# Kernel tuning notes

Hardware: AMD Instinct MI355X
Metric: run time of the kernel (lower is better)

The kernel has to match this reference:

```python
import jax, jax.numpy as jnp
import numpy as np

BATCH, SEQ, H_IN, N_STATE, H_OUT = 16, 4096, 128, 256, 128
RMIN, RMAX, MAX_PHASE = 0.9, 1.0, 6.283


def setup_inputs() -> dict:
    key = jax.random.key(0)
    ks = jax.random.split(key, 9)
    u = jax.random.normal(ks[0], (BATCH, SEQ, H_IN), jnp.float32)
    # LRU exponential parameterization init (matches torch __init__)
    u1 = jax.random.uniform(ks[1], (N_STATE,), jnp.float32)
    u2 = jax.random.uniform(ks[2], (N_STATE,), jnp.float32)
    nu_log = jnp.log(-0.5 * jnp.log(u1 * (RMAX + RMIN) * (RMAX - RMIN) + RMIN ** 2))
    theta_log = jnp.log(MAX_PHASE * u2)
    lam_abs = jnp.exp(-jnp.exp(nu_log))
    gamma_log = jnp.log(jnp.sqrt(1.0 - lam_abs ** 2))
    s2in = np.sqrt(2.0 * H_IN).astype(np.float32)
    B_re = jax.random.normal(ks[3], (N_STATE, H_IN), jnp.float32) / s2in
    B_im = jax.random.normal(ks[4], (N_STATE, H_IN), jnp.float32) / s2in
    sst = np.sqrt(float(N_STATE)).astype(np.float32)
    C_re = jax.random.normal(ks[5], (H_OUT, N_STATE), jnp.float32) / sst
    C_im = jax.random.normal(ks[6], (H_OUT, N_STATE), jnp.float32) / sst
    D = jax.random.normal(ks[7], (H_OUT, H_IN), jnp.float32) / np.sqrt(float(H_IN)).astype(np.float32)
    return dict(u=u, nu_log=nu_log, theta_log=theta_log, gamma_log=gamma_log,
                B_re=B_re, B_im=B_im, C_re=C_re, C_im=C_im, D=D)


def _combine(a, b):
    # complex affine composition: (l, x) o (l', x') -> (l*l', l'*x + x')
    l1r, l1i, x1r, x1i = a
    l2r, l2i, x2r, x2i = b
    lr = l1r * l2r - l1i * l2i
    li = l1r * l2i + l1i * l2r
    xr = l2r * x1r - l2i * x1i + x2r
    xi = l2r * x1i + l2i * x1r + x2i
    return (lr, li, xr, xi)


def reference(u, nu_log, theta_log, gamma_log, B_re, B_im, C_re, C_im, D):
    lam_mod = jnp.exp(-jnp.exp(nu_log))          # |lambda|, [N]
    th = jnp.exp(theta_log)
    lam_re = lam_mod * jnp.cos(th)
    lam_im = lam_mod * jnp.sin(th)
    gammas = jnp.exp(gamma_log)                  # [N]
    # input projection Bu_t = gamma * (B @ u_t), complex -> real/imag parts
    Bu_re = jnp.einsum('blh,nh->bln', u, B_re) * gammas  # [B,L,N]
    Bu_im = jnp.einsum('blh,nh->bln', u, B_im) * gammas
    Bsz, L, N = Bu_re.shape
    lr = jnp.broadcast_to(lam_re, (Bsz, L, N))
    li = jnp.broadcast_to(lam_im, (Bsz, L, N))
    # parallel scan of x_t = lambda * x_{t-1} + Bu_t, x0 = 0
    _, _, xr, xi = jax.lax.associative_scan(_combine, (lr, li, Bu_re, Bu_im), axis=1)
    zero = jnp.zeros((Bsz, 1, N), u.dtype)
    pre_re = jnp.concatenate([zero, xr[:, :-1]], axis=1)  # states[:, :-1]
    pre_im = jnp.concatenate([zero, xi[:, :-1]], axis=1)
    # y_t = Re(C x_{t-1}) + D u_t
    y = (jnp.einsum('bln,on->blo', pre_re, C_re)
         - jnp.einsum('bln,on->blo', pre_im, C_im)
         + jnp.einsum('blh,oh->blo', u, D))
    return y
```

## Files before the change

### kernel.cpp

```cpp
#include <hip/hip_runtime.h>
#include <math.h>

#define BATCH 16
#define SEQ   4096
#define HIN   128
#define NST   256
#define HOUT  128
#define CL    32
#define NC    (SEQ/CL)
#define ROWS  (BATCH*SEQ)
#define KTOT  640
#define NPRE  512

typedef __attribute__((ext_vector_type(8))) short short8;
typedef __attribute__((ext_vector_type(4))) float f32x4;

__device__ inline unsigned short f2bf(float f) {
  union { float f; unsigned u; } v; v.f = f;
  unsigned r = v.u + 0x7FFFu + ((v.u >> 16) & 1u);
  return (unsigned short)(r >> 16);
}
__device__ inline float bf2f(unsigned short s) {
  union { unsigned u; float f; } v; v.u = ((unsigned)s) << 16;
  return v.f;
}
__device__ inline float bits2f(unsigned u) {
  union { unsigned u; float f; } v; v.u = u; return v.f;
}

__global__ __launch_bounds__(256) void k_prep(
    const float* __restrict__ nu_log, const float* __restrict__ theta_log,
    const float* __restrict__ gamma_log,
    const float* __restrict__ Bre, const float* __restrict__ Bim,
    const float* __restrict__ Cre, const float* __restrict__ Cim,
    const float* __restrict__ Dm,
    float* __restrict__ lamre, float* __restrict__ lamim,
    unsigned* __restrict__ lamPk,
    unsigned short* __restrict__ Wb, unsigned short* __restrict__ W) {
  int idx = blockIdx.x*256 + threadIdx.x;
  if (idx < NST) {
    float lm = expf(-expf(nu_log[idx]));
    float th = expf(theta_log[idx]);
    float lr = lm * cosf(th), li = lm * sinf(th);
    lamre[idx] = lr; lamim[idx] = li;
    float pr = 1.f, pi = 0.f;
    for (int j = 0; j < CL; ++j) {
      lamPk[j*NST + idx] = ((unsigned)f2bf(pi) << 16) | (unsigned)f2bf(pr);
      float nr = pr*lr - pi*li;
      float ni = pr*li + pi*lr;
      pr = nr; pi = ni;
    }
  }
  if (idx < 512*HIN) {
    int r = idx >> 7, h = idx & 127;
    int g = r >> 7;
    int w = r & 127;
    int n = g*64 + (w & 63);
    float gm = expf(gamma_log[n]);
    float v = (w < 64) ? Bre[n*HIN + h] : Bim[n*HIN + h];
    Wb[idx] = f2bf(gm * v);
  }
  if (idx < HOUT*KTOT) {
    int o = idx / KTOT, k = idx - o*KTOT;
    float v;
    if (k < NST)        v =  Cre[o*NST + k];
    else if (k < 2*NST) v = -Cim[o*NST + (k - NST)];
    else                v =  Dm[o*HIN + (k - 2*NST)];
    W[idx] = f2bf(v);
  }
}

union SharedBu {
  unsigned short B[128][136];
  float stg[2][32][132];
};
__global__ __launch_bounds__(256) void k_bu(
    const float* __restrict__ u, const unsigned short* __restrict__ Wb,
    const float* __restrict__ lamre, const float* __restrict__ lamim,
    unsigned short* __restrict__ preL,
    float* __restrict__ S_re, float* __restrict__ S_im) {
  __shared__ unsigned short Asl[128][136];
  __shared__ SharedBu sh;
  int tid = threadIdx.x;
  int row0 = blockIdx.x * 128;
  int wid = tid >> 6, lane = tid & 63;
  int lm = lane & 15, lq = lane >> 4;
  int m0 = (wid >> 1) * 64, n0 = (wid & 1) * 64;
  int b = row0 >> 12;
  int cbase = (row0 & 4095) >> 5;
#pragma unroll
  for (int cc = 0; cc < 8; ++cc) {
    int ch = cc*256 + tid;
    int r = ch >> 4, h0 = (ch & 15) * 8;
    const float* src = u + (size_t)(row0 + r)*HIN + h0;
    float4 v0 = *(const float4*)src;
    float4 v1 = *(const float4*)(src + 4);
    unsigned short o[8];
    o[0]=f2bf(v0.x); o[1]=f2bf(v0.y); o[2]=f2bf(v0.z); o[3]=f2bf(v0.w);
    o[4]=f2bf(v1.x); o[5]=f2bf(v1.y); o[6]=f2bf(v1.z); o[7]=f2bf(v1.w);
    *(short8*)&Asl[r][h0] = *(const short8*)o;
  }
  for (int g = 0; g < 4; ++g) {
    __syncthreads();
#pragma unroll
    for (int cc = 0; cc < 8; ++cc) {
      int ch = cc*256 + tid;
      int r = ch >> 4, h0 = (ch & 15) * 8;
      *(short8*)&sh.B[r][h0] = *(const short8*)&Wb[(size_t)(g*128 + r)*HIN + h0];
    }
    __syncthreads();
    f32x4 acc[4][4];
#pragma unroll
    for (int i = 0; i < 4; ++i)
#pragma unroll
      for (int j = 0; j < 4; ++j) acc[i][j] = (f32x4)0.f;
#pragma unroll
    for (int ks = 0; ks < 4; ++ks) {
      int k0 = ks*32 + lq*8;
      short8 a[4], bb[4];
#pragma unroll
      for (int i = 0; i < 4; ++i) a[i] = *(const short8*)&Asl[m0 + i*16 + lm][k0];
#pragma unroll
      for (int j = 0; j < 4; ++j) bb[j] = *(const short8*)&sh.B[n0 + j*16 + lm][k0];
#pragma unroll
      for (int i = 0; i < 4; ++i)
#pragma unroll
        for (int j = 0; j < 4; ++j)
          acc[i][j] = __builtin_amdgcn_mfma_f32_16x16x32_bf16(a[i], bb[j], acc[i][j], 0, 0, 0);
    }
    for (int p = 0; p < 2; ++p) {
      __syncthreads();
#pragma unroll
      for (int ii = 0; ii < 2; ++ii) {
        int i = 2*p + ii;
#pragma unroll
        for (int j = 0; j < 4; ++j)
#pragma unroll
          for (int r = 0; r < 4; ++r) {
            int trow = ii*16 + lq*4 + r;
            sh.stg[wid >> 1][trow][n0 + j*16 + lm] = acc[i][j][r];
          }
      }
      __syncthreads();
      if (tid < 128) {
        int buf = tid >> 6, nl = tid & 63;
        int ng = g*64 + nl;
        float lr = lamre[ng], li = lamim[ng];
        float rr[CL], ri[CL];
#pragma unroll
        for (int t = 0; t < CL; ++t) {
          rr[t] = sh.stg[buf][t][nl];
          ri[t] = sh.stg[buf][t][64 + nl];
        }
        int rowb = row0 + buf*64 + p*32;
        unsigned short* pl = preL + (size_t)rowb*NPRE;
        float sr = 0.f, si = 0.f;
#pragma unroll
        for (int t = 0; t < CL; ++t) {
          pl[ng]       = f2bf(sr);
          pl[NST + ng] = f2bf(si);
          float nr = lr*sr - li*si + rr[t];
          float ni = lr*si + li*sr + ri[t];
          sr = nr; si = ni; pl += NPRE;
        }
        int c = cbase + buf*2 + p;
        int idx = (b*NC + c)*NST + ng;
        S_re[idx] = sr; S_im[idx] = si;
      }
    }
  }
}

__global__ __launch_bounds__(256) void k_carry2(
    const float* __restrict__ S_re, const float* __restrict__ S_im,
    const float* __restrict__ lamre, const float* __restrict__ lamim,
    float* __restrict__ G_re, float* __restrict__ G_im) {
  int blk = blockIdx.x;
  int b = blk >> 3, g = blk & 7;
  int n = threadIdx.x;
  float ar = lamre[n], ai = lamim[n];
#pragma unroll
  for (int s = 0; s < 5; ++s) { float nr = ar*ar - ai*ai, ni = 2.f*ar*ai; ar = nr; ai = ni; }
  float tr = 0.f, ti = 0.f;
#pragma unroll
  for (int cc = 0; cc < 16; ++cc) {
    int idx = (b*NC + g*16 + cc)*NST + n;
    float nr = ar*tr - ai*ti + S_re[idx];
    float ni = ar*ti + ai*tr + S_im[idx];
    tr = nr; ti = ni;
  }
  int gi = (b*8 + g)*NST + n;
  G_re[gi] = tr; G_im[gi] = ti;
}

__global__ __launch_bounds__(256) void k_final(
    const float* __restrict__ S_re, const float* __restrict__ S_im,
    const float* __restrict__ G_re, const float* __restrict__ G_im,
    const float* __restrict__ lamre, const float* __restrict__ lamim,
    unsigned* __restrict__ X0Pk) {
  int blk = blockIdx.x;
  int b = blk >> 3, g = blk & 7;
  int n = threadIdx.x;
  float ar = lamre[n], ai = lamim[n];
#pragma unroll
  for (int s = 0; s < 5; ++s) { float nr = ar*ar - ai*ai, ni = 2.f*ar*ai; ar = nr; ai = ni; }
  float a5r = ar, a5i = ai;
#pragma unroll
  for (int s = 0; s < 4; ++s) { float nr = a5r*a5r - a5i*a5i, ni = 2.f*a5r*a5i; a5r = nr; a5i = ni; }
  float pr = 0.f, pi = 0.f;
  for (int j = 0; j < g; ++j) {
    int gi = (b*8 + j)*NST + n;
    float nr = a5r*pr - a5i*pi + G_re[gi];
    float ni = a5r*pi + a5i*pr + G_im[gi];
    pr = nr; pi = ni;
  }
  float xr = pr, xi = pi;
#pragma unroll
  for (int cc = 0; cc < 16; ++cc) {
    int idx = (b*NC + g*16 + cc)*NST + n;
    X0Pk[idx] = ((unsigned)f2bf(xi) << 16) | (unsigned)f2bf(xr);
    float nr = ar*xr - ai*xi + S_re[idx];
    float ni = ar*xi + ai*xr + S_im[idx];
    xr = nr; xi = ni;
  }
}

__global__ __launch_bounds__(256) void k_out2(
    const unsigned short* __restrict__ preL, const float* __restrict__ u,
    const unsigned short* __restrict__ W,
    const unsigned* __restrict__ lamPk, const unsigned* __restrict__ X0Pk,
    float* __restrict__ y) {
  __shared__ unsigned short Bsl[128][136];
  int tid = threadIdx.x;
  int row0 = blockIdx.x * 128;
  int wid = tid >> 6, lane = tid & 63;
  int lm = lane & 15, lq = lane >> 4;
  int m0 = wid * 32;
  f32x4 acc[2][8];
#pragma unroll
  for (int i = 0; i < 2; ++i)
#pragma unroll
    for (int j = 0; j < 8; ++j) acc[i][j] = (f32x4)0.f;
  int grow[2];
  grow[0] = row0 + m0 + lm;
  grow[1] = grow[0] + 16;
  for (int s = 0; s < 5; ++s) {
#pragma unroll
    for (int cc = 0; cc < 8; ++cc) {
      int ch = cc*256 + tid;
      int r = ch >> 4, h0 = (ch & 15) * 8;
      *(short8*)&Bsl[r][h0] = *(const short8*)&W[(size_t)r*KTOT + s*128 + h0];
    }
    __syncthreads();
#pragma unroll
    for (int ks = 0; ks < 4; ++ks) {
      int k0 = ks*32 + lq*8;
      short8 a[2];
      if (s < 4) {
        int n = ((s & 1) << 7) + k0;
#pragma unroll
        for (int i = 0; i < 2; ++i) {
          int gr = grow[i];
          int j32 = gr & 31, cidx = gr >> 5;
          short8 loc = *(const short8*)&preL[(size_t)gr*NPRE + s*128 + k0];
          uint4 lp0 = *(const uint4*)&lamPk[j32*NST + n];
          uint4 lp1 = *(const uint4*)&lamPk[j32*NST + n + 4];
          uint4 xp0 = *(const uint4*)&X0Pk[cidx*NST + n];
          uint4 xp1 = *(const uint4*)&X0Pk[cidx*NST + n + 4];
          unsigned lps[8] = {lp0.x, lp0.y, lp0.z, lp0.w, lp1.x, lp1.y, lp1.z, lp1.w};
          unsigned xps[8] = {xp0.x, xp0.y, xp0.z, xp0.w, xp1.x, xp1.y, xp1.z, xp1.w};
          unsigned short o[8];
#pragma unroll
          for (int e = 0; e < 8; ++e) {
            float lr = bits2f(lps[e] << 16);
            float li = bits2f(lps[e] & 0xFFFF0000u);
            float xr = bits2f(xps[e] << 16);
            float xi = bits2f(xps[e] & 0xFFFF0000u);
            float lv = bf2f((unsigned short)loc[e]);
            float v = (s < 2) ? (lv + lr*xr - li*xi)
                              : (lv + lr*xi + li*xr);
            o[e] = f2bf(v);
          }
          a[i] = *(const short8*)o;
        }
      } else {
#pragma unroll
        for (int i = 0; i < 2; ++i) {
          const float* src = u + (size_t)grow[i]*HIN + k0;
          float4 v0 = *(const float4*)src;
          float4 v1 = *(const float4*)(src + 4);
          unsigned short o[8];
          o[0]=f2bf(v0.x); o[1]=f2bf(v0.y); o[2]=f2bf(v0.z); o[3]=f2bf(v0.w);
          o[4]=f2bf(v1.x); o[5]=f2bf(v1.y); o[6]=f2bf(v1.z); o[7]=f2bf(v1.w);
          a[i] = *(const short8*)o;
        }
      }
      short8 bb[8];
#pragma unroll
      for (int j = 0; j < 8; ++j) bb[j] = *(const short8*)&Bsl[j*16 + lm][k0];
#pragma unroll
      for (int i = 0; i < 2; ++i)
#pragma unroll
        for (int j = 0; j < 8; ++j)
          acc[i][j] = __builtin_amdgcn_mfma_f32_16x16x32_bf16(a[i], bb[j], acc[i][j], 0, 0, 0);
    }
    __syncthreads();
  }
#pragma unroll
  for (int i = 0; i < 2; ++i)
#pragma unroll
    for (int j = 0; j < 8; ++j)
#pragma unroll
      for (int r = 0; r < 4; ++r)
        y[(size_t)(row0 + m0 + i*16 + lq*4 + r)*HOUT + j*16 + lm] = acc[i][j][r];
}

extern "C" void kernel_launch(void* const* d_in, const int* in_sizes, int n_in,
                              void* d_out, int out_size, void* d_ws, size_t ws_size,
                              hipStream_t stream) {
  const float* u         = (const float*)d_in[0];
  const float* nu_log    = (const float*)d_in[1];
  const float* theta_log = (const float*)d_in[2];
  const float* gamma_log = (const float*)d_in[3];
  const float* B_re      = (const float*)d_in[4];
  const float* B_im      = (const float*)d_in[5];
  const float* C_re      = (const float*)d_in[6];
  const float* C_im      = (const float*)d_in[7];
  const float* Dm        = (const float*)d_in[8];
  float* y = (float*)d_out;
  char* ws = (char*)d_ws;

  size_t off = 0;
  float* lamre = (float*)(ws + off);            off += 1024;
  float* lamim = (float*)(ws + off);            off += 1024;
  unsigned* lamPk = (unsigned*)(ws + off);      off += 32768;
  unsigned short* Wb = (unsigned short*)(ws + off); off += 131072;
  unsigned short* W  = (unsigned short*)(ws + off); off += 163840;
  unsigned short* preL = (unsigned short*)(ws + off); off += (size_t)ROWS*NPRE*2;
  float* S_re = (float*)(ws + off);             off += 2097152;
  float* S_im = (float*)(ws + off);             off += 2097152;
  float* G_re = (float*)(ws + off);             off += 131072;
  float* G_im = (float*)(ws + off);             off += 131072;
  unsigned* X0Pk = (unsigned*)(ws + off);       off += 2097152;

  k_prep<<<320, 256, 0, stream>>>(nu_log, theta_log, gamma_log, B_re, B_im,
                                  C_re, C_im, Dm, lamre, lamim, lamPk, Wb, W);
  k_bu<<<ROWS/128, 256, 0, stream>>>(u, Wb, lamre, lamim, preL, S_re, S_im);
  k_carry2<<<BATCH*8, 256, 0, stream>>>(S_re, S_im, lamre, lamim, G_re, G_im);
  k_final<<<BATCH*8, 256, 0, stream>>>(S_re, S_im, G_re, G_im, lamre, lamim, X0Pk);
  k_out2<<<ROWS/128, 256, 0, stream>>>(preL, u, W, lamPk, X0Pk, y);
}
```

Baseline: 173.3 us.

## Halve row tiles in Bu and output GEMMs, add occupancy bounds, prefetch carry loads

Both GEMM kernels now process 64 rows per block instead of 128. That doubles the grid and cuts the accumulator registers per wave. Launch-bounds hints ask for 3 and 4 blocks per CU, aiming for more waves to hide memory latency. The carry and final scan kernels now load their S and G values into registers before the serial recurrence, so the loads are no longer interleaved with the dependent math. The cost is that each block now reloads the full weight tile for half as much output, so weight traffic from LDS and global memory per row doubles.

```diff
diff --git a/kernel.cpp b/kernel.cpp
--- a/kernel.cpp
+++ b/kernel.cpp
@@ -74,22 +74,23 @@
   unsigned short B[128][136];
   float stg[2][32][132];
 };
-__global__ __launch_bounds__(256) void k_bu(
+__global__ __launch_bounds__(256, 3) void k_bu(
     const float* __restrict__ u, const unsigned short* __restrict__ Wb,
     const float* __restrict__ lamre, const float* __restrict__ lamim,
     unsigned short* __restrict__ preL,
     float* __restrict__ S_re, float* __restrict__ S_im) {
-  __shared__ unsigned short Asl[128][136];
+  __shared__ unsigned short Asl[64][136];
   __shared__ SharedBu sh;
   int tid = threadIdx.x;
-  int row0 = blockIdx.x * 128;
+  int row0 = blockIdx.x * 64;
   int wid = tid >> 6, lane = tid & 63;
   int lm = lane & 15, lq = lane >> 4;
-  int m0 = (wid >> 1) * 64, n0 = (wid & 1) * 64;
+  int m0 = (wid >> 1) * 32, n0 = (wid & 1) * 64;
+  int ck = wid >> 1;
   int b = row0 >> 12;
   int cbase = (row0 & 4095) >> 5;
 #pragma unroll
-  for (int cc = 0; cc < 8; ++cc) {
+  for (int cc = 0; cc < 4; ++cc) {
     int ch = cc*256 + tid;
     int r = ch >> 4, h0 = (ch & 15) * 8;
     const float* src = u + (size_t)(row0 + r)*HIN + h0;
@@ -109,64 +110,60 @@
       *(short8*)&sh.B[r][h0] = *(const short8*)&Wb[(size_t)(g*128 + r)*HIN + h0];
     }
     __syncthreads();
-    f32x4 acc[4][4];
-#pragma unroll
-    for (int i = 0; i < 4; ++i)
+    f32x4 acc[2][4];
+#pragma unroll
+    for (int i = 0; i < 2; ++i)
 #pragma unroll
       for (int j = 0; j < 4; ++j) acc[i][j] = (f32x4)0.f;
 #pragma unroll
     for (int ks = 0; ks < 4; ++ks) {
       int k0 = ks*32 + lq*8;
-      short8 a[4], bb[4];
-#pragma unroll
-      for (int i = 0; i < 4; ++i) a[i] = *(const short8*)&Asl[m0 + i*16 + lm][k0];
+      short8 a[2], bb[4];
+#pragma unroll
+      for (int i = 0; i < 2; ++i) a[i] = *(const short8*)&Asl[m0 + i*16 + lm][k0];
 #pragma unroll
       for (int j = 0; j < 4; ++j) bb[j] = *(const short8*)&sh.B[n0 + j*16 + lm][k0];
 #pragma unroll
-      for (int i = 0; i < 4; ++i)
+      for (int i = 0; i < 2; ++i)
 #pragma unroll
         for (int j = 0; j < 4; ++j)
           acc[i][j] = __builtin_amdgcn_mfma_f32_16x16x32_bf16(a[i], bb[j], acc[i][j], 0, 0, 0);
     }
-    for (int p = 0; p < 2; ++p) {
-      __syncthreads();
-#pragma unroll
-      for (int ii = 0; ii < 2; ++ii) {
-        int i = 2*p + ii;
-#pragma unroll
-        for (int j = 0; j < 4; ++j)
-#pragma unroll
-          for (int r = 0; r < 4; ++r) {
-            int trow = ii*16 + lq*4 + r;
-            sh.stg[wid >> 1][trow][n0 + j*16 + lm] = acc[i][j][r];
-          }
+    __syncthreads();
+#pragma unroll
+    for (int i = 0; i < 2; ++i)
+#pragma unroll
+      for (int j = 0; j < 4; ++j)
+#pragma unroll
+        for (int r = 0; r < 4; ++r) {
+          int trow = i*16 + lq*4 + r;
+          sh.stg[ck][trow][n0 + j*16 + lm] = acc[i][j][r];
+        }
+    __syncthreads();
+    if (tid < 128) {
+      int buf = tid >> 6, nl = tid & 63;
+      int ng = g*64 + nl;
+      float lr = lamre[ng], li = lamim[ng];
+      float rr[CL], ri[CL];
+#pragma unroll
+      for (int t = 0; t < CL; ++t) {
+        rr[t] = sh.stg[buf][t][nl];
+        ri[t] = sh.stg[buf][t][64 + nl];
       }
-      __syncthreads();
-      if (tid < 128) {
-        int buf = tid >> 6, nl = tid & 63;
-        int ng = g*64 + nl;
-        float lr = lamre[ng], li = lamim[ng];
-        float rr[CL], ri[CL];
-#pragma unroll
-        for (int t = 0; t < CL; ++t) {
-          rr[t] = sh.stg[buf][t][nl];
-          ri[t] = sh.stg[buf][t][64 + nl];
-        }
-        int rowb = row0 + buf*64 + p*32;
-        unsigned short* pl = preL + (size_t)rowb*NPRE;
-        float sr = 0.f, si = 0.f;
-#pragma unroll
-        for (int t = 0; t < CL; ++t) {
-          pl[ng]       = f2bf(sr);
-          pl[NST + ng] = f2bf(si);
-          float nr = lr*sr - li*si + rr[t];
-          float ni = lr*si + li*sr + ri[t];
-          sr = nr; si = ni; pl += NPRE;
-        }
-        int c = cbase + buf*2 + p;
-        int idx = (b*NC + c)*NST + ng;
-        S_re[idx] = sr; S_im[idx] = si;
+      int rowb = row0 + buf*32;
+      unsigned short* pl = preL + (size_t)rowb*NPRE;
+      float sr = 0.f, si = 0.f;
+#pragma unroll
+      for (int t = 0; t < CL; ++t) {
+        pl[ng]       = f2bf(sr);
+        pl[NST + ng] = f2bf(si);
+        float nr = lr*sr - li*si + rr[t];
+        float ni = lr*si + li*sr + ri[t];
+        sr = nr; si = ni; pl += NPRE;
       }
+      int c = cbase + buf;
+      int idx = (b*NC + c)*NST + ng;
+      S_re[idx] = sr; S_im[idx] = si;
     }
   }
 }
@@ -181,12 +178,17 @@
   float ar = lamre[n], ai = lamim[n];
 #pragma unroll
   for (int s = 0; s < 5; ++s) { float nr = ar*ar - ai*ai, ni = 2.f*ar*ai; ar = nr; ai = ni; }
-  float tr = 0.f, ti = 0.f;
+  float sre[16], sim[16];
 #pragma unroll
   for (int cc = 0; cc < 16; ++cc) {
     int idx = (b*NC + g*16 + cc)*NST + n;
-    float nr = ar*tr - ai*ti + S_re[idx];
-    float ni = ar*ti + ai*tr + S_im[idx];
+    sre[cc] = S_re[idx]; sim[cc] = S_im[idx];
+  }
+  float tr = 0.f, ti = 0.f;
+#pragma unroll
+  for (int cc = 0; cc < 16; ++cc) {
+    float nr = ar*tr - ai*ti + sre[cc];
+    float ni = ar*ti + ai*tr + sim[cc];
     tr = nr; ti = ni;
   }
   int gi = (b*8 + g)*NST + n;
@@ -207,43 +209,54 @@
   float a5r = ar, a5i = ai;
 #pragma unroll
   for (int s = 0; s < 4; ++s) { float nr = a5r*a5r - a5i*a5i, ni = 2.f*a5r*a5i; a5r = nr; a5i = ni; }
+  float gr_[7], gi_[7];
+#pragma unroll
+  for (int j = 0; j < 7; ++j) {
+    if (j < g) { int gi2 = (b*8 + j)*NST + n; gr_[j] = G_re[gi2]; gi_[j] = G_im[gi2]; }
+    else       { gr_[j] = 0.f; gi_[j] = 0.f; }
+  }
   float pr = 0.f, pi = 0.f;
-  for (int j = 0; j < g; ++j) {
-    int gi = (b*8 + j)*NST + n;
-    float nr = a5r*pr - a5i*pi + G_re[gi];
-    float ni = a5r*pi + a5i*pr + G_im[gi];
-    pr = nr; pi = ni;
+#pragma unroll
+  for (int j = 0; j < 7; ++j) {
+    if (j < g) {
+      float nr = a5r*pr - a5i*pi + gr_[j];
+      float ni = a5r*pi + a5i*pr + gi_[j];
+      pr = nr; pi = ni;
+    }
+  }
+  float sre[16], sim[16];
+#pragma unroll
+  for (int cc = 0; cc < 16; ++cc) {
+    int idx = (b*NC + g*16 + cc)*NST + n;
+    sre[cc] = S_re[idx]; sim[cc] = S_im[idx];
   }
   float xr = pr, xi = pi;
 #pragma unroll
   for (int cc = 0; cc < 16; ++cc) {
     int idx = (b*NC + g*16 + cc)*NST + n;
     X0Pk[idx] = ((unsigned)f2bf(xi) << 16) | (unsigned)f2bf(xr);
-    float nr = ar*xr - ai*xi + S_re[idx];
-    float ni = ar*xi + ai*xr + S_im[idx];
+    float nr = ar*xr - ai*xi + sre[cc];
+    float ni = ar*xi + ai*xr + sim[cc];
     xr = nr; xi = ni;
   }
 }
 
-__global__ __launch_bounds__(256) void k_out2(
+__global__ __launch_bounds__(256, 4) void k_out2(
     const unsigned short* __restrict__ preL, const float* __restrict__ u,
     const unsigned short* __restrict__ W,
     const unsigned* __restrict__ lamPk, const unsigned* __restrict__ X0Pk,
     float* __restrict__ y) {
   __shared__ unsigned short Bsl[128][136];
   int tid = threadIdx.x;
-  int row0 = blockIdx.x * 128;
+  int row0 = blockIdx.x * 64;
   int wid = tid >> 6, lane = tid & 63;
   int lm = lane & 15, lq = lane >> 4;
-  int m0 = wid * 32;
-  f32x4 acc[2][8];
-#pragma unroll
-  for (int i = 0; i < 2; ++i)
-#pragma unroll
-    for (int j = 0; j < 8; ++j) acc[i][j] = (f32x4)0.f;
-  int grow[2];
-  grow[0] = row0 + m0 + lm;
-  grow[1] = grow[0] + 16;
+  int m0 = wid * 16;
+  f32x4 acc[8];
+#pragma unroll
+  for (int j = 0; j < 8; ++j) acc[j] = (f32x4)0.f;
+  int grow = row0 + m0 + lm;
+  int j32 = grow & 31, cidx = grow >> 5;
   for (int s = 0; s < 5; ++s) {
 #pragma unroll
     for (int cc = 0; cc < 8; ++cc) {
@@ -255,64 +268,52 @@
 #pragma unroll
     for (int ks = 0; ks < 4; ++ks) {
       int k0 = ks*32 + lq*8;
-      short8 a[2];
+      short8 a;
       if (s < 4) {
         int n = ((s & 1) << 7) + k0;
-#pragma unroll
-        for (int i = 0; i < 2; ++i) {
-          int gr = grow[i];
-          int j32 = gr & 31, cidx = gr >> 5;
-          short8 loc = *(const short8*)&preL[(size_t)gr*NPRE + s*128 + k0];
-          uint4 lp0 = *(const uint4*)&lamPk[j32*NST + n];
-          uint4 lp1 = *(const uint4*)&lamPk[j32*NST + n + 4];
-          uint4 xp0 = *(const uint4*)&X0Pk[cidx*NST + n];
-          uint4 xp1 = *(const uint4*)&X0Pk[cidx*NST + n + 4];
-          unsigned lps[8] = {lp0.x, lp0.y, lp0.z, lp0.w, lp1.x, lp1.y, lp1.z, lp1.w};
-          unsigned xps[8] = {xp0.x, xp0.y, xp0.z, xp0.w, xp1.x, xp1.y, xp1.z, xp1.w};
-          unsigned short o[8];
-#pragma unroll
-          for (int e = 0; e < 8; ++e) {
-            float lr = bits2f(lps[e] << 16);
-            float li = bits2f(lps[e] & 0xFFFF0000u);
-            float xr = bits2f(xps[e] << 16);
-            float xi = bits2f(xps[e] & 0xFFFF0000u);
-            float lv = bf2f((unsigned short)loc[e]);
-            float v = (s < 2) ? (lv + lr*xr - li*xi)
-                              : (lv + lr*xi + li*xr);
-            o[e] = f2bf(v);
-          }
-          a[i] = *(const short8*)o;
+        short8 loc = *(const short8*)&preL[(size_t)grow*NPRE + s*128 + k0];
+        uint4 lp0 = *(const uint4*)&lamPk[j32*NST + n];
+        uint4 lp1 = *(const uint4*)&lamPk[j32*NST + n + 4];
+        uint4 xp0 = *(const uint4*)&X0Pk[cidx*NST + n];
+        uint4 xp1 = *(const uint4*)&X0Pk[cidx*NST + n + 4];
+        unsigned lps[8] = {lp0.x, lp0.y, lp0.z, lp0.w, lp1.x, lp1.y, lp1.z, lp1.w};
+        unsigned xps[8] = {xp0.x, xp0.y, xp0.z, xp0.w, xp1.x, xp1.y, xp1.z, xp1.w};
+        unsigned short o[8];
+#pragma unroll
+        for (int e = 0; e < 8; ++e) {
+          float lr = bits2f(lps[e] << 16);
+          float li = bits2f(lps[e] & 0xFFFF0000u);
+          float xr = bits2f(xps[e] << 16);
+          float xi = bits2f(xps[e] & 0xFFFF0000u);
+          float lv = bf2f((unsigned short)loc[e]);
+          float v = (s < 2) ? (lv + lr*xr - li*xi)
+                            : (lv + lr*xi + li*xr);
+          o[e] = f2bf(v);
         }
+        a = *(const short8*)o;
       } else {
-#pragma unroll
-        for (int i = 0; i < 2; ++i) {
-          const float* src = u + (size_t)grow[i]*HIN + k0;
-          float4 v0 = *(const float4*)src;
-          float4 v1 = *(const float4*)(src + 4);
-          unsigned short o[8];
-          o[0]=f2bf(v0.x); o[1]=f2bf(v0.y); o[2]=f2bf(v0.z); o[3]=f2bf(v0.w);
-          o[4]=f2bf(v1.x); o[5]=f2bf(v1.y); o[6]=f2bf(v1.z); o[7]=f2bf(v1.w);
-          a[i] = *(const short8*)o;
-        }
+        const float* src = u + (size_t)grow*HIN + k0;
+        float4 v0 = *(const float4*)src;
+        float4 v1 = *(const float4*)(src + 4);
+        unsigned short o[8];
+        o[0]=f2bf(v0.x); o[1]=f2bf(v0.y); o[2]=f2bf(v0.z); o[3]=f2bf(v0.w);
+        o[4]=f2bf(v1.x); o[5]=f2bf(v1.y); o[6]=f2bf(v1.z); o[7]=f2bf(v1.w);
+        a = *(const short8*)o;
       }
       short8 bb[8];
 #pragma unroll
       for (int j = 0; j < 8; ++j) bb[j] = *(const short8*)&Bsl[j*16 + lm][k0];
 #pragma unroll
-      for (int i = 0; i < 2; ++i)
-#pragma unroll
-        for (int j = 0; j < 8; ++j)
-          acc[i][j] = __builtin_amdgcn_mfma_f32_16x16x32_bf16(a[i], bb[j], acc[i][j], 0, 0, 0);
-    }
-    __syncthreads();
-  }
-#pragma unroll
-  for (int i = 0; i < 2; ++i)
-#pragma unroll
-    for (int j = 0; j < 8; ++j)
-#pragma unroll
-      for (int r = 0; r < 4; ++r)
-        y[(size_t)(row0 + m0 + i*16 + lq*4 + r)*HOUT + j*16 + lm] = acc[i][j][r];
+      for (int j = 0; j < 8; ++j)
+        acc[j] = __builtin_amdgcn_mfma_f32_16x16x32_bf16(a, bb[j], acc[j], 0, 0, 0);
+    }
+    __syncthreads();
+  }
+#pragma unroll
+  for (int j = 0; j < 8; ++j)
+#pragma unroll
+    for (int r = 0; r < 4; ++r)
+      y[(size_t)(row0 + m0 + lq*4 + r)*HOUT + j*16 + lm] = acc[j][r];
 }
 
 extern "C" void kernel_launch(void* const* d_in, const int* in_sizes, int n_in,
@@ -345,8 +346,8 @@
 
   k_prep<<<320, 256, 0, stream>>>(nu_log, theta_log, gamma_log, B_re, B_im,
                                   C_re, C_im, Dm, lamre, lamim, lamPk, Wb, W);
-  k_bu<<<ROWS/128, 256, 0, stream>>>(u, Wb, lamre, lamim, preL, S_re, S_im);
+  k_bu<<<ROWS/64, 256, 0, stream>>>(u, Wb, lamre, lamim, preL, S_re, S_im);
   k_carry2<<<BATCH*8, 256, 0, stream>>>(S_re, S_im, lamre, lamim, G_re, G_im);
   k_final<<<BATCH*8, 256, 0, stream>>>(S_re, S_im, G_re, G_im, lamre, lamim, X0Pk);
-  k_out2<<<ROWS/128, 256, 0, stream>>>(preL, u, W, lamPk, X0Pk, y);
-}
+  k_out2<<<ROWS/64, 256, 0, stream>>>(preL, u, W, lamPk, X0Pk, y);
+}
```

After: 178.1 us. 2.8% more time.

## Stage A operand tile in LDS in output GEMM and batch scan loads

Applied to the files above, without the earlier changes.

The output GEMM kernel now builds the full 128x128 A tile (state reconstruction from local prefix, lambda powers and chunk carries, or bf16-converted u) cooperatively into shared memory with coalesced row-contiguous loads. Previously each wave gathered its A fragments directly from global memory in MFMA layout. The carry and final scan kernels also preload all S/G values into registers before the serial recurrence, so loads are issued together instead of inside the dependent chain. The cost is an extra 34KB of LDS per block, which may reduce occupancy, plus an extra LDS round trip for A.

```diff
diff --git a/kernel.cpp b/kernel.cpp
--- a/kernel.cpp
+++ b/kernel.cpp
@@ -181,12 +181,17 @@
   float ar = lamre[n], ai = lamim[n];
 #pragma unroll
   for (int s = 0; s < 5; ++s) { float nr = ar*ar - ai*ai, ni = 2.f*ar*ai; ar = nr; ai = ni; }
-  float tr = 0.f, ti = 0.f;
+  float sre[16], sim[16];
 #pragma unroll
   for (int cc = 0; cc < 16; ++cc) {
     int idx = (b*NC + g*16 + cc)*NST + n;
-    float nr = ar*tr - ai*ti + S_re[idx];
-    float ni = ar*ti + ai*tr + S_im[idx];
+    sre[cc] = S_re[idx]; sim[cc] = S_im[idx];
+  }
+  float tr = 0.f, ti = 0.f;
+#pragma unroll
+  for (int cc = 0; cc < 16; ++cc) {
+    float nr = ar*tr - ai*ti + sre[cc];
+    float ni = ar*ti + ai*tr + sim[cc];
     tr = nr; ti = ni;
   }
   int gi = (b*8 + g)*NST + n;
@@ -207,20 +212,34 @@
   float a5r = ar, a5i = ai;
 #pragma unroll
   for (int s = 0; s < 4; ++s) { float nr = a5r*a5r - a5i*a5i, ni = 2.f*a5r*a5i; a5r = nr; a5i = ni; }
+  float gr_[7], gi_[7];
+#pragma unroll
+  for (int j = 0; j < 7; ++j) {
+    if (j < g) { int gi2 = (b*8 + j)*NST + n; gr_[j] = G_re[gi2]; gi_[j] = G_im[gi2]; }
+    else       { gr_[j] = 0.f; gi_[j] = 0.f; }
+  }
   float pr = 0.f, pi = 0.f;
-  for (int j = 0; j < g; ++j) {
-    int gi = (b*8 + j)*NST + n;
-    float nr = a5r*pr - a5i*pi + G_re[gi];
-    float ni = a5r*pi + a5i*pr + G_im[gi];
-    pr = nr; pi = ni;
+#pragma unroll
+  for (int j = 0; j < 7; ++j) {
+    if (j < g) {
+      float nr = a5r*pr - a5i*pi + gr_[j];
+      float ni = a5r*pi + a5i*pr + gi_[j];
+      pr = nr; pi = ni;
+    }
+  }
+  float sre[16], sim[16];
+#pragma unroll
+  for (int cc = 0; cc < 16; ++cc) {
+    int idx = (b*NC + g*16 + cc)*NST + n;
+    sre[cc] = S_re[idx]; sim[cc] = S_im[idx];
   }
   float xr = pr, xi = pi;
 #pragma unroll
   for (int cc = 0; cc < 16; ++cc) {
     int idx = (b*NC + g*16 + cc)*NST + n;
     X0Pk[idx] = ((unsigned)f2bf(xi) << 16) | (unsigned)f2bf(xr);
-    float nr = ar*xr - ai*xi + S_re[idx];
-    float ni = ar*xi + ai*xr + S_im[idx];
+    float nr = ar*xr - ai*xi + sre[cc];
+    float ni = ar*xi + ai*xr + sim[cc];
     xr = nr; xi = ni;
   }
 }
@@ -230,6 +249,7 @@
     const unsigned short* __restrict__ W,
     const unsigned* __restrict__ lamPk, const unsigned* __restrict__ X0Pk,
     float* __restrict__ y) {
+  __shared__ unsigned short Asl[128][136];
   __shared__ unsigned short Bsl[128][136];
   int tid = threadIdx.x;
   int row0 = blockIdx.x * 128;
@@ -241,61 +261,65 @@
   for (int i = 0; i < 2; ++i)
 #pragma unroll
     for (int j = 0; j < 8; ++j) acc[i][j] = (f32x4)0.f;
-  int grow[2];
-  grow[0] = row0 + m0 + lm;
-  grow[1] = grow[0] + 16;
   for (int s = 0; s < 5; ++s) {
+    __syncthreads();
 #pragma unroll
     for (int cc = 0; cc < 8; ++cc) {
       int ch = cc*256 + tid;
       int r = ch >> 4, h0 = (ch & 15) * 8;
       *(short8*)&Bsl[r][h0] = *(const short8*)&W[(size_t)r*KTOT + s*128 + h0];
     }
+    if (s < 4) {
+#pragma unroll
+      for (int cc = 0; cc < 8; ++cc) {
+        int ch = cc*256 + tid;
+        int r = ch >> 4, h0 = (ch & 15) * 8;
+        int grow = row0 + r;
+        int j32 = r & 31;
+        int cidx = grow >> 5;
+        int n = ((s & 1) << 7) + h0;
+        short8 loc = *(const short8*)&preL[(size_t)grow*NPRE + s*128 + h0];
+        uint4 lp0 = *(const uint4*)&lamPk[j32*NST + n];
+        uint4 lp1 = *(const uint4*)&lamPk[j32*NST + n + 4];
+        uint4 xp0 = *(const uint4*)&X0Pk[(size_t)cidx*NST + n];
+        uint4 xp1 = *(const uint4*)&X0Pk[(size_t)cidx*NST + n + 4];
+        unsigned lps[8] = {lp0.x, lp0.y, lp0.z, lp0.w, lp1.x, lp1.y, lp1.z, lp1.w};
+        unsigned xps[8] = {xp0.x, xp0.y, xp0.z, xp0.w, xp1.x, xp1.y, xp1.z, xp1.w};
+        unsigned short o[8];
+#pragma unroll
+        for (int e = 0; e < 8; ++e) {
+          float lr = bits2f(lps[e] << 16);
+          float li = bits2f(lps[e] & 0xFFFF0000u);
+          float xr = bits2f(xps[e] << 16);
+          float xi = bits2f(xps[e] & 0xFFFF0000u);
+          float lv = bf2f((unsigned short)loc[e]);
+          float v = (s < 2) ? (lv + lr*xr - li*xi)
+                            : (lv + lr*xi + li*xr);
+          o[e] = f2bf(v);
+        }
+        *(short8*)&Asl[r][h0] = *(const short8*)o;
+      }
+    } else {
+#pragma unroll
+      for (int cc = 0; cc < 8; ++cc) {
+        int ch = cc*256 + tid;
+        int r = ch >> 4, h0 = (ch & 15) * 8;
+        const float* src = u + (size_t)(row0 + r)*HIN + h0;
+        float4 v0 = *(const float4*)src;
+        float4 v1 = *(const float4*)(src + 4);
+        unsigned short o[8];
+        o[0]=f2bf(v0.x); o[1]=f2bf(v0.y); o[2]=f2bf(v0.z); o[3]=f2bf(v0.w);
+        o[4]=f2bf(v1.x); o[5]=f2bf(v1.y); o[6]=f2bf(v1.z); o[7]=f2bf(v1.w);
+        *(short8*)&Asl[r][h0] = *(const short8*)o;
+      }
+    }
     __syncthreads();
 #pragma unroll
     for (int ks = 0; ks < 4; ++ks) {
       int k0 = ks*32 + lq*8;
-      short8 a[2];
-      if (s < 4) {
-        int n = ((s & 1) << 7) + k0;
-#pragma unroll
-        for (int i = 0; i < 2; ++i) {
-          int gr = grow[i];
-          int j32 = gr & 31, cidx = gr >> 5;
-          short8 loc = *(const short8*)&preL[(size_t)gr*NPRE + s*128 + k0];
-          uint4 lp0 = *(const uint4*)&lamPk[j32*NST + n];
-          uint4 lp1 = *(const uint4*)&lamPk[j32*NST + n + 4];
-          uint4 xp0 = *(const uint4*)&X0Pk[cidx*NST + n];
-          uint4 xp1 = *(const uint4*)&X0Pk[cidx*NST + n + 4];
-          unsigned lps[8] = {lp0.x, lp0.y, lp0.z, lp0.w, lp1.x, lp1.y, lp1.z, lp1.w};
-          unsigned xps[8] = {xp0.x, xp0.y, xp0.z, xp0.w, xp1.x, xp1.y, xp1.z, xp1.w};
-          unsigned short o[8];
-#pragma unroll
-          for (int e = 0; e < 8; ++e) {
-            float lr = bits2f(lps[e] << 16);
-            float li = bits2f(lps[e] & 0xFFFF0000u);
-            float xr = bits2f(xps[e] << 16);
-            float xi = bits2f(xps[e] & 0xFFFF0000u);
-            float lv = bf2f((unsigned short)loc[e]);
-            float v = (s < 2) ? (lv + lr*xr - li*xi)
-                              : (lv + lr*xi + li*xr);
-            o[e] = f2bf(v);
-          }
-          a[i] = *(const short8*)o;
-        }
-      } else {
-#pragma unroll
-        for (int i = 0; i < 2; ++i) {
-          const float* src = u + (size_t)grow[i]*HIN + k0;
-          float4 v0 = *(const float4*)src;
-          float4 v1 = *(const float4*)(src + 4);
-          unsigned short o[8];
-          o[0]=f2bf(v0.x); o[1]=f2bf(v0.y); o[2]=f2bf(v0.z); o[3]=f2bf(v0.w);
-          o[4]=f2bf(v1.x); o[5]=f2bf(v1.y); o[6]=f2bf(v1.z); o[7]=f2bf(v1.w);
-          a[i] = *(const short8*)o;
-        }
-      }
-      short8 bb[8];
+      short8 a[2], bb[8];
+#pragma unroll
+      for (int i = 0; i < 2; ++i) a[i] = *(const short8*)&Asl[m0 + i*16 + lm][k0];
 #pragma unroll
       for (int j = 0; j < 8; ++j) bb[j] = *(const short8*)&Bsl[j*16 + lm][k0];
 #pragma unroll
@@ -304,7 +328,6 @@
         for (int j = 0; j < 8; ++j)
           acc[i][j] = __builtin_amdgcn_mfma_f32_16x16x32_bf16(a[i], bb[j], acc[i][j], 0, 0, 0);
     }
-    __syncthreads();
   }
 #pragma unroll
   for (int i = 0; i < 2; ++i)
```

After: 162.9 us. 1.06x faster.
